# Performance work log

Hardware: AMD Instinct MI355X
Metric: run time of the kernel (lower is better)

## Reference

```python
import jax, jax.numpy as jnp
import numpy as np

NUM_HEADS = 16
EMBED_DIM = 1024
HEAD_SIZE = EMBED_DIM // NUM_HEADS


def setup_inputs() -> dict:
    key = jax.random.key(0)
    ks = jax.random.split(key, 9)
    B, S, D = 4, 2048, EMBED_DIM
    scale = 1.0 / np.sqrt(D)
    x = jax.random.normal(ks[0], (B, S, D), dtype=jnp.float32)
    Wq = jax.random.normal(ks[1], (D, D), dtype=jnp.float32) * scale
    bq = jnp.zeros((D,), dtype=jnp.float32)
    Wk = jax.random.normal(ks[2], (D, D), dtype=jnp.float32) * scale
    bk = jnp.zeros((D,), dtype=jnp.float32)
    Wv = jax.random.normal(ks[3], (D, D), dtype=jnp.float32) * scale
    bv = jnp.zeros((D,), dtype=jnp.float32)
    Wo = jax.random.normal(ks[4], (D, D), dtype=jnp.float32) * scale
    bo = jnp.zeros((D,), dtype=jnp.float32)
    return {"x": x, "Wq": Wq, "bq": bq, "Wk": Wk, "bk": bk,
            "Wv": Wv, "bv": bv, "Wo": Wo, "bo": bo}


def reference(x, Wq, bq, Wk, bk, Wv, bv, Wo, bo):
    B, S, D = x.shape
    H, Hd = NUM_HEADS, HEAD_SIZE

    def split_heads(t):  # [B,S,D] -> [B,H,S,Hd]
        return t.reshape(B, S, H, Hd).transpose(0, 2, 1, 3)

    q = split_heads(x @ Wq + bq)
    k = split_heads(x @ Wk + bk)
    v = split_heads(x @ Wv + bv)

    scores = jnp.einsum("bhqd,bhkd->bhqk", q, k) / np.sqrt(Hd)
    probs = jax.nn.softmax(scores, axis=-1)  # dropout rate=0 -> identity
    ctx = jnp.einsum("bhqk,bhkd->bhqd", probs, v)
    ctx = ctx.transpose(0, 2, 1, 3).reshape(B, S, D)
    return ctx @ Wo + bo
```

## Files before the change

kernel.cpp:

```cpp
#include <hip/hip_runtime.h>
#include <cstdint>


typedef unsigned short ushort_t;
typedef __attribute__((ext_vector_type(8))) short short8;
typedef __attribute__((ext_vector_type(4))) float f32x4;

constexpr int Bn = 4, Sn = 2048, Dn = 1024, Hn = 16;
constexpr int Mn = Bn * Sn;
constexpr float QSCALE = 0.125f * 1.44269504088896340736f;

__device__ __forceinline__ ushort_t f2b(float f) {
    union { float f; unsigned u; } v; v.f = f;
    unsigned u = v.u;
    return (ushort_t)((u + 0x7fffu + ((u >> 16) & 1u)) >> 16);
}

__device__ __forceinline__ unsigned cvt_pk_bf16(float lo, float hi) {
    unsigned r;
    asm("v_cvt_pk_bf16_f32 %0, %1, %2" : "=v"(r) : "v"(lo), "v"(hi));
    return r;
}

__device__ __forceinline__ float exp2_hw(float x) {
    float y;
    asm("v_exp_f32 %0, %1" : "=v"(y) : "v"(x));
    return y;
}

__device__ __forceinline__ void gl_lds16(const void* g, void* l) {
    __builtin_amdgcn_global_load_lds(
        (const __attribute__((address_space(1))) unsigned int*)g,
        (__attribute__((address_space(3))) unsigned int*)l, 16, 0, 0);
}

__global__ void cast_f32_bf16(const float* __restrict__ in, ushort_t* __restrict__ out, int n4) {
    int i = blockIdx.x * blockDim.x + threadIdx.x;
    if (i < n4) {
        float4 f = ((const float4*)in)[i];
        ushort4 o;
        o.x = f2b(f.x); o.y = f2b(f.y); o.z = f2b(f.z); o.w = f2b(f.w);
        ((ushort4*)out)[i] = o;
    }
}

__global__ void transpose_cast_w4(
    const float* __restrict__ W0, const float* __restrict__ W1,
    const float* __restrict__ W2, const float* __restrict__ W3,
    ushort_t* __restrict__ T0, ushort_t* __restrict__ T1,
    ushort_t* __restrict__ T2, ushort_t* __restrict__ T3, int dim) {
    __shared__ float tile[32][33];
    int z = blockIdx.z;
    const float* W = z == 0 ? W0 : (z == 1 ? W1 : (z == 2 ? W2 : W3));
    ushort_t* Wt = z == 0 ? T0 : (z == 1 ? T1 : (z == 2 ? T2 : T3));
    int bx = blockIdx.x * 32;
    int by = blockIdx.y * 32;
    int tx = threadIdx.x, ty = threadIdx.y;
    for (int i = 0; i < 32; i += 8)
        tile[ty + i][tx] = W[(size_t)(by + ty + i) * dim + bx + tx];
    __syncthreads();
    for (int i = 0; i < 32; i += 8)
        Wt[(size_t)(bx + ty + i) * dim + by + tx] = f2b(tile[tx][ty + i]);
}

template <int OUTF32, int QKVSEL>
__global__ __launch_bounds__(256) void gemm_bt(
    const ushort_t* __restrict__ A, const ushort_t* __restrict__ Bt,
    const float* __restrict__ b0, const float* __restrict__ b1, const float* __restrict__ b2,
    void* __restrict__ Cv, ushort_t* __restrict__ Vt,
    int Mq, int Nq, int Kq, float osc0, int nbx) {
    alignas(16) __shared__ ushort_t Al[128 * 64];
    alignas(16) __shared__ ushort_t Bl[128 * 64];
    const int tid = threadIdx.x;
    const int l = tid & 63, wid = tid >> 6;
    const int lo = l & 15, g = l >> 4;
    const int wm = wid >> 1, wn = wid & 1;
    const int per_xcd = (int)gridDim.x >> 3;
    const int virt = ((int)blockIdx.x & 7) * per_xcd + ((int)blockIdx.x >> 3);
    const int m0 = (virt / nbx) * 128, n0g = (virt % nbx) * 128;
    int sel = QKVSEL ? (n0g >> 10) : 0;
    const float* bias = QKVSEL ? (sel == 0 ? b0 : (sel == 1 ? b1 : b2)) : b0;
    float oscale = (QKVSEL && sel != 0) ? 1.0f : osc0;
    const int n0 = QKVSEL ? (n0g & 1023) : n0g;

    const int rr = l >> 3, cc = l & 7;

    f32x4 acc[4][4];
    for (int a = 0; a < 4; ++a)
        for (int b = 0; b < 4; ++b) acc[a][b] = f32x4{0.f, 0.f, 0.f, 0.f};

    for (int kt = 0; kt < Kq; kt += 64) {
        __syncthreads();
#pragma unroll
        for (int i = 0; i < 4; ++i) {
            int row = wid * 32 + i * 8 + rr;
            gl_lds16(&A[(size_t)(m0 + row) * Kq + kt + cc * 8], &Al[(wid * 32 + i * 8) * 64]);
            gl_lds16(&Bt[(size_t)(n0g + row) * Kq + kt + cc * 8], &Bl[(wid * 32 + i * 8) * 64]);
        }
        __syncthreads();
#pragma unroll
        for (int ks = 0; ks < 2; ++ks) {
            short8 af[4], bf[4];
#pragma unroll
            for (int mi = 0; mi < 4; ++mi)
                af[mi] = *(const short8*)&Al[(wm * 64 + mi * 16 + lo) * 64 + ks * 32 + g * 8];
#pragma unroll
            for (int ni = 0; ni < 4; ++ni)
                bf[ni] = *(const short8*)&Bl[(wn * 64 + ni * 16 + lo) * 64 + ks * 32 + g * 8];
            __builtin_amdgcn_s_setprio(1);
#pragma unroll
            for (int mi = 0; mi < 4; ++mi)
#pragma unroll
                for (int ni = 0; ni < 4; ++ni)
                    acc[mi][ni] = __builtin_amdgcn_mfma_f32_16x16x32_bf16(af[mi], bf[ni], acc[mi][ni], 0, 0, 0);
            __builtin_amdgcn_s_setprio(0);
        }
    }
    for (int mi = 0; mi < 4; ++mi) {
        int row = m0 + wm * 64 + mi * 16 + g * 4;
        for (int ni = 0; ni < 4; ++ni) {
            int col = n0 + wn * 64 + ni * 16 + lo;
            float bcol = bias ? bias[col] : 0.f;
            float v0 = (acc[mi][ni][0] + bcol) * oscale;
            float v1 = (acc[mi][ni][1] + bcol) * oscale;
            float v2 = (acc[mi][ni][2] + bcol) * oscale;
            float v3 = (acc[mi][ni][3] + bcol) * oscale;
            if (OUTF32) {
                ((float*)Cv)[(size_t)(row + 0) * Nq + col] = v0;
                ((float*)Cv)[(size_t)(row + 1) * Nq + col] = v1;
                ((float*)Cv)[(size_t)(row + 2) * Nq + col] = v2;
                ((float*)Cv)[(size_t)(row + 3) * Nq + col] = v3;
            } else if (QKVSEL && sel == 2) {
                size_t drow = (size_t)((((unsigned)row >> 11) << 4) + ((unsigned)col >> 6)) * 64 + (col & 63);
                uint2 w;
                w.x = cvt_pk_bf16(v0, v1);
                w.y = cvt_pk_bf16(v2, v3);
                *(uint2*)&Vt[drow * Sn + (row & 2047)] = w;
            } else {
                ushort_t* out = (ushort_t*)Cv + (size_t)sel * Mn * Dn;
                out[(size_t)(row + 0) * Nq + col] = f2b(v0);
                out[(size_t)(row + 1) * Nq + col] = f2b(v1);
                out[(size_t)(row + 2) * Nq + col] = f2b(v2);
                out[(size_t)(row + 3) * Nq + col] = f2b(v3);
            }
        }
    }
}

__global__ __launch_bounds__(256, 2) void attn_kernel(
    const ushort_t* __restrict__ Qg, const ushort_t* __restrict__ Kg,
    const ushort_t* __restrict__ Vtg, ushort_t* __restrict__ Ctx) {
    alignas(16) __shared__ ushort_t Kl[2][64 * 64];
    alignas(16) __shared__ ushort_t Vl[2][64 * 64];
    alignas(16) __shared__ ushort_t Pl[4][64 * 64];
    const int tid = threadIdx.x;
    const int l = tid & 63, wid = tid >> 6;
    const int lo = l & 15, g = l >> 4;
    const int virt = (blockIdx.x & 7) * 64 + (blockIdx.x >> 3);
    const int bh = virt >> 3, qc = virt & 7;
    const int b = bh >> 4, h = bh & 15;
    const int q0 = qc * 256 + wid * 64;
    constexpr int NT = Sn / 64;

    short8 qf[4][2];
#pragma unroll
    for (int qi = 0; qi < 4; ++qi) {
        size_t qrow = (size_t)(b * Sn + q0 + qi * 16 + lo);
#pragma unroll
        for (int ks = 0; ks < 2; ++ks)
            qf[qi][ks] = *(const short8*)&Qg[qrow * Dn + h * 64 + ks * 32 + g * 8];
    }

    const int rr = l >> 3, cc = l & 7;
    const int swc = ((cc ^ rr) << 4);
    const char* gK = (const char*)(Kg + (size_t)(b * Sn) * Dn + h * 64);
    const char* gV = (const char*)(Vtg + (size_t)(bh * 64) * Sn);

    float ls[4] = {0.f, 0.f, 0.f, 0.f};
    f32x4 ctx[4][4];
#pragma unroll
    for (int qi = 0; qi < 4; ++qi)
#pragma unroll
        for (int ni = 0; ni < 4; ++ni) ctx[qi][ni] = f32x4{0.f, 0.f, 0.f, 0.f};

    char* Pw = (char*)Pl[wid];

#define STAGE_KV(T, BUF)                                                                 \
    {                                                                                    \
        int row = wid * 8 + rr;                                                          \
        gl_lds16(gK + ((size_t)((T)*64 + row) * Dn) * 2 + swc,                           \
                 &Kl[BUF][(wid * 8) * 64]);                                              \
        gl_lds16(gK + ((size_t)((T)*64 + row + 32) * Dn) * 2 + swc,                      \
                 &Kl[BUF][(wid * 8 + 32) * 64]);                                         \
        gl_lds16(gV + ((size_t)row * Sn + (size_t)(T)*64) * 2 + swc,                     \
                 &Vl[BUF][(wid * 8) * 64]);                                              \
        gl_lds16(gV + ((size_t)(row + 32) * Sn + (size_t)(T)*64) * 2 + swc,              \
                 &Vl[BUF][(wid * 8 + 32) * 64]);                                         \
    }

    STAGE_KV(0, 0);

    for (int t = 0; t < NT; ++t) {
        const char* Kb = (const char*)Kl[t & 1];
        const char* Vb = (const char*)Vl[t & 1];
        asm volatile("s_waitcnt vmcnt(0)" ::: "memory");
        __builtin_amdgcn_s_barrier();
        __builtin_amdgcn_sched_barrier(0);
        if (t + 1 < NT) STAGE_KV(t + 1, (t + 1) & 1);

        f32x4 sa[4][4];
#pragma unroll
        for (int qi = 0; qi < 4; ++qi)
#pragma unroll
            for (int ni = 0; ni < 4; ++ni) sa[qi][ni] = f32x4{0.f, 0.f, 0.f, 0.f};
#pragma unroll
        for (int ks = 0; ks < 2; ++ks) {
            short8 kf[4];
#pragma unroll
            for (int ni = 0; ni < 4; ++ni) {
                int row = ni * 16 + lo;
                kf[ni] = *(const short8*)(Kb + ((row * 128 + ks * 64 + g * 16) ^ ((lo & 7) << 4)));
            }
            __builtin_amdgcn_s_setprio(1);
#pragma unroll
            for (int qi = 0; qi < 4; ++qi)
#pragma unroll
                for (int ni = 0; ni < 4; ++ni)
                    sa[qi][ni] = __builtin_amdgcn_mfma_f32_16x16x32_bf16(kf[ni], qf[qi][ks], sa[qi][ni], 0, 0, 0);
            __builtin_amdgcn_s_setprio(0);
        }

        short8 vf[2][4];
#pragma unroll
        for (int ks = 0; ks < 2; ++ks)
#pragma unroll
            for (int ni = 0; ni < 4; ++ni) {
                int row = ni * 16 + lo;
                vf[ks][ni] = *(const short8*)(Vb + ((row * 128 + ks * 64 + g * 16) ^ ((lo & 7) << 4)));
            }

#pragma unroll
        for (int qi = 0; qi < 4; ++qi) {
            float r0 = 0.f, r1 = 0.f, r2 = 0.f, r3 = 0.f;
#pragma unroll
            for (int i = 0; i < 4; ++i) {
                sa[qi][0][i] = exp2_hw(sa[qi][0][i]); r0 += sa[qi][0][i];
                sa[qi][1][i] = exp2_hw(sa[qi][1][i]); r1 += sa[qi][1][i];
                sa[qi][2][i] = exp2_hw(sa[qi][2][i]); r2 += sa[qi][2][i];
                sa[qi][3][i] = exp2_hw(sa[qi][3][i]); r3 += sa[qi][3][i];
            }
            ls[qi] += (r0 + r1) + (r2 + r3);
#pragma unroll
            for (int ni = 0; ni < 4; ++ni) {
                uint2 w;
                w.x = cvt_pk_bf16(sa[qi][ni][0], sa[qi][ni][1]);
                w.y = cvt_pk_bf16(sa[qi][ni][2], sa[qi][ni][3]);
                unsigned byte = (unsigned)(((qi * 16 + lo) * 128 + (ni * 16 + g * 4) * 2) ^ ((lo & 7) << 4));
                *(uint2*)(Pw + byte) = w;
            }
        }
        asm volatile("s_waitcnt lgkmcnt(0)" ::: "memory");
        __builtin_amdgcn_sched_barrier(0);

        short8 pa[4][2];
#pragma unroll
        for (int qi = 0; qi < 4; ++qi)
#pragma unroll
            for (int ks = 0; ks < 2; ++ks)
                pa[qi][ks] = *(const short8*)(Pw + (((qi * 16 + lo) * 128 + ks * 64 + g * 16) ^ ((lo & 7) << 4)));
        __builtin_amdgcn_s_setprio(1);
#pragma unroll
        for (int ks = 0; ks < 2; ++ks)
#pragma unroll
            for (int qi = 0; qi < 4; ++qi)
#pragma unroll
                for (int ni = 0; ni < 4; ++ni)
                    ctx[qi][ni] = __builtin_amdgcn_mfma_f32_16x16x32_bf16(pa[qi][ks], vf[ks][ni], ctx[qi][ni], 0, 0, 0);
        __builtin_amdgcn_s_setprio(0);
    }
#undef STAGE_KV

#pragma unroll
    for (int qi = 0; qi < 4; ++qi) {
        float lsum = ls[qi];
        lsum += __shfl_xor(lsum, 16);
        lsum += __shfl_xor(lsum, 32);
        float linv = 1.0f / lsum;
#pragma unroll
        for (int i = 0; i < 4; ++i) {
            float lrow = __shfl(linv, g * 4 + i);
            int prow = qi * 16 + g * 4 + i;
#pragma unroll
            for (int ni = 0; ni < 4; ++ni) {
                unsigned byte = (unsigned)((prow * 128 + (ni * 16 + lo) * 2) ^ ((prow & 7) << 4));
                *(ushort_t*)(Pw + byte) = f2b(ctx[qi][ni][i] * lrow);
            }
        }
    }
    asm volatile("s_waitcnt lgkmcnt(0)" ::: "memory");
    __builtin_amdgcn_sched_barrier(0);
#pragma unroll
    for (int j = 0; j < 8; ++j) {
        int row = j * 8 + rr;
        uint4 w = *(const uint4*)(Pw + ((row * 128 + cc * 16) ^ ((row & 7) << 4)));
        *(uint4*)&Ctx[(size_t)(b * Sn + q0 + row) * Dn + h * 64 + cc * 8] = w;
    }
}

extern "C" void kernel_launch(void* const* d_in, const int* in_sizes, int n_in,
                              void* d_out, int out_size, void* d_ws, size_t ws_size,
                              hipStream_t stream) {
    const float* x  = (const float*)d_in[0];
    const float* Wq = (const float*)d_in[1];
    const float* bq = (const float*)d_in[2];
    const float* Wk = (const float*)d_in[3];
    const float* bk = (const float*)d_in[4];
    const float* Wv = (const float*)d_in[5];
    const float* bv = (const float*)d_in[6];
    const float* Wo = (const float*)d_in[7];
    const float* bo = (const float*)d_in[8];

    ushort_t* ws = (ushort_t*)d_ws;
    const size_t MD = (size_t)Mn * Dn;
    const size_t DD = (size_t)Dn * Dn;
    ushort_t* xb  = ws;
    ushort_t* wqt = xb + MD;
    ushort_t* wkt = wqt + DD;
    ushort_t* wvt = wkt + DD;
    ushort_t* wot = wvt + DD;
    ushort_t* qb  = wot + DD;
    ushort_t* kb  = qb + MD;
    ushort_t* vb  = kb + MD;
    ushort_t* vt  = vb + MD;
    ushort_t* cx  = vt + MD;

    int n4 = (int)(MD / 4);
    cast_f32_bf16<<<(n4 + 255) / 256, 256, 0, stream>>>(x, xb, n4);
    transpose_cast_w4<<<dim3(Dn / 32, Dn / 32, 4), dim3(32, 8), 0, stream>>>(
        Wq, Wk, Wv, Wo, wqt, wkt, wvt, wot, Dn);
    gemm_bt<0, 1><<<dim3(1536), 256, 0, stream>>>(
        xb, wqt, bq, bk, bv, qb, vt, Mn, Dn, Dn, QSCALE, 24);
    attn_kernel<<<dim3(512), 256, 0, stream>>>(qb, kb, vt, cx);
    gemm_bt<1, 0><<<dim3(512), 256, 0, stream>>>(
        cx, wot, bo, nullptr, nullptr, (float*)d_out, nullptr, Mn, Dn, Dn, 1.0f, 8);
}
```

Measured before the change: 197.7 us.

## Software-pipeline QK^T of next KV tile with softmax and PV of current tile

Restructures the attention inner loop so that the QK^T MFMAs and V-fragment loads for tile t+1 are issued between the exp/bf16-pack of tile t and its PV MFMAs. The loop is manually unrolled by two with ping-pong score and V-fragment register sets, and KV prefetch is moved two tiles ahead. The aim is to overlap transcendental/VALU softmax work with matrix-core work and hide the LDS latency that the old serial per-tile schedule exposed. In exchange it doubles the live score accumulators and V fragments, which raises VGPR pressure and may reduce occupancy or cause spills. It also assumes NT is even.

Measured after the change: 638.4 us. 223% more time.

```diff
diff --git a/kernel.cpp b/kernel.cpp
--- a/kernel.cpp
+++ b/kernel.cpp
@@ -185,6 +185,9 @@
 
     char* Pw = (char*)Pl[wid];
 
+    f32x4 sa0[4][4], sa1[4][4];
+    short8 vf0[2][4], vf1[2][4];
+
 #define STAGE_KV(T, BUF)                                                                 \
     {                                                                                    \
         int row = wid * 8 + rr;                                                          \
@@ -198,86 +201,103 @@
                  &Vl[BUF][(wid * 8 + 32) * 64]);                                         \
     }
 
+#define QK_VF(BUF, SAN, VFN)                                                             \
+    {                                                                                    \
+        const char* Kb_ = (const char*)Kl[BUF];                                          \
+        const char* Vb_ = (const char*)Vl[BUF];                                          \
+        _Pragma("unroll")                                                                \
+        for (int qi = 0; qi < 4; ++qi)                                                   \
+            _Pragma("unroll")                                                            \
+            for (int ni = 0; ni < 4; ++ni) SAN[qi][ni] = f32x4{0.f, 0.f, 0.f, 0.f};      \
+        _Pragma("unroll")                                                                \
+        for (int ks = 0; ks < 2; ++ks) {                                                 \
+            short8 kf[4];                                                                \
+            _Pragma("unroll")                                                            \
+            for (int ni = 0; ni < 4; ++ni) {                                             \
+                int row = ni * 16 + lo;                                                  \
+                kf[ni] = *(const short8*)(Kb_ + ((row * 128 + ks * 64 + g * 16) ^ ((lo & 7) << 4))); \
+            }                                                                            \
+            __builtin_amdgcn_s_setprio(1);                                               \
+            _Pragma("unroll")                                                            \
+            for (int qi = 0; qi < 4; ++qi)                                               \
+                _Pragma("unroll")                                                        \
+                for (int ni = 0; ni < 4; ++ni)                                           \
+                    SAN[qi][ni] = __builtin_amdgcn_mfma_f32_16x16x32_bf16(kf[ni], qf[qi][ks], SAN[qi][ni], 0, 0, 0); \
+            __builtin_amdgcn_s_setprio(0);                                               \
+        }                                                                                \
+        _Pragma("unroll")                                                                \
+        for (int ks = 0; ks < 2; ++ks)                                                   \
+            _Pragma("unroll")                                                            \
+            for (int ni = 0; ni < 4; ++ni) {                                             \
+                int row = ni * 16 + lo;                                                  \
+                VFN[ks][ni] = *(const short8*)(Vb_ + ((row * 128 + ks * 64 + g * 16) ^ ((lo & 7) << 4))); \
+            }                                                                            \
+    }
+
+#define BODY(T, SAC, VFC, SAN, VFN, CB, NB)                                              \
+    {                                                                                    \
+                          \
+        _Pragma("unroll")                                                                \
+        for (int qi = 0; qi < 4; ++qi) {                                                 \
+            float r0 = 0.f, r1 = 0.f, r2 = 0.f, r3 = 0.f;                                \
+            _Pragma("unroll")                                                            \
+            for (int i = 0; i < 4; ++i) {                                                \
+                SAC[qi][0][i] = exp2_hw(SAC[qi][0][i]); r0 += SAC[qi][0][i];             \
+                SAC[qi][1][i] = exp2_hw(SAC[qi][1][i]); r1 += SAC[qi][1][i];             \
+                SAC[qi][2][i] = exp2_hw(SAC[qi][2][i]); r2 += SAC[qi][2][i];             \
+                SAC[qi][3][i] = exp2_hw(SAC[qi][3][i]); r3 += SAC[qi][3][i];             \
+            }                                                                            \
+            ls[qi] += (r0 + r1) + (r2 + r3);                                             \
+            _Pragma("unroll")                                                            \
+            for (int ni = 0; ni < 4; ++ni) {                                             \
+                uint2 w;                                                                 \
+                w.x = cvt_pk_bf16(SAC[qi][ni][0], SAC[qi][ni][1]);                       \
+                w.y = cvt_pk_bf16(SAC[qi][ni][2], SAC[qi][ni][3]);                       \
+                unsigned byte = (unsigned)(((qi * 16 + lo) * 128 + (ni * 16 + g * 4) * 2) ^ ((lo & 7) << 4)); \
+                *(uint2*)(Pw + byte) = w;                                                \
+            }                                                                            \
+        }                                                                                \
+        if ((T) + 1 < NT) {                                                              \
+            asm volatile("s_waitcnt vmcnt(0)" ::: "memory");      \
+            __builtin_amdgcn_s_barrier();     \
+            __builtin_amdgcn_sched_barrier(0);                                           \
+            if ((T) + 2 < NT) STAGE_KV((T) + 2, CB);                                     \
+            QK_VF(NB, SAN, VFN);                                  \
+        }                                                                                \
+                  \
+        asm volatile("s_waitcnt lgkmcnt(0)" ::: "memory");                               \
+        __builtin_amdgcn_sched_barrier(0);                                               \
+        short8 pa[4][2];                                                                 \
+        _Pragma("unroll")                                                                \
+        for (int qi = 0; qi < 4; ++qi)                                                   \
+            _Pragma("unroll")                                                            \
+            for (int ks = 0; ks < 2; ++ks)                                               \
+                pa[qi][ks] = *(const short8*)(Pw + (((qi * 16 + lo) * 128 + ks * 64 + g * 16) ^ ((lo & 7) << 4))); \
+        __builtin_amdgcn_s_setprio(1);                                                   \
+        _Pragma("unroll")                                                                \
+        for (int ks = 0; ks < 2; ++ks)                                                   \
+            _Pragma("unroll")                                                            \
+            for (int qi = 0; qi < 4; ++qi)                                               \
+                _Pragma("unroll")                                                        \
+                for (int ni = 0; ni < 4; ++ni)                                           \
+                    ctx[qi][ni] = __builtin_amdgcn_mfma_f32_16x16x32_bf16(pa[qi][ks], VFC[ks][ni], ctx[qi][ni], 0, 0, 0); \
+        __builtin_amdgcn_s_setprio(0);                                                   \
+    }
+
     STAGE_KV(0, 0);
-
-    for (int t = 0; t < NT; ++t) {
-        const char* Kb = (const char*)Kl[t & 1];
-        const char* Vb = (const char*)Vl[t & 1];
-        asm volatile("s_waitcnt vmcnt(0)" ::: "memory");
-        __builtin_amdgcn_s_barrier();
-        __builtin_amdgcn_sched_barrier(0);
-        if (t + 1 < NT) STAGE_KV(t + 1, (t + 1) & 1);
-
-        f32x4 sa[4][4];
-#pragma unroll
-        for (int qi = 0; qi < 4; ++qi)
-#pragma unroll
-            for (int ni = 0; ni < 4; ++ni) sa[qi][ni] = f32x4{0.f, 0.f, 0.f, 0.f};
-#pragma unroll
-        for (int ks = 0; ks < 2; ++ks) {
-            short8 kf[4];
-#pragma unroll
-            for (int ni = 0; ni < 4; ++ni) {
-                int row = ni * 16 + lo;
-                kf[ni] = *(const short8*)(Kb + ((row * 128 + ks * 64 + g * 16) ^ ((lo & 7) << 4)));
-            }
-            __builtin_amdgcn_s_setprio(1);
-#pragma unroll
-            for (int qi = 0; qi < 4; ++qi)
-#pragma unroll
-                for (int ni = 0; ni < 4; ++ni)
-                    sa[qi][ni] = __builtin_amdgcn_mfma_f32_16x16x32_bf16(kf[ni], qf[qi][ks], sa[qi][ni], 0, 0, 0);
-            __builtin_amdgcn_s_setprio(0);
-        }
-
-        short8 vf[2][4];
-#pragma unroll
-        for (int ks = 0; ks < 2; ++ks)
-#pragma unroll
-            for (int ni = 0; ni < 4; ++ni) {
-                int row = ni * 16 + lo;
-                vf[ks][ni] = *(const short8*)(Vb + ((row * 128 + ks * 64 + g * 16) ^ ((lo & 7) << 4)));
-            }
-
-#pragma unroll
-        for (int qi = 0; qi < 4; ++qi) {
-            float r0 = 0.f, r1 = 0.f, r2 = 0.f, r3 = 0.f;
-#pragma unroll
-            for (int i = 0; i < 4; ++i) {
-                sa[qi][0][i] = exp2_hw(sa[qi][0][i]); r0 += sa[qi][0][i];
-                sa[qi][1][i] = exp2_hw(sa[qi][1][i]); r1 += sa[qi][1][i];
-                sa[qi][2][i] = exp2_hw(sa[qi][2][i]); r2 += sa[qi][2][i];
-                sa[qi][3][i] = exp2_hw(sa[qi][3][i]); r3 += sa[qi][3][i];
-            }
-            ls[qi] += (r0 + r1) + (r2 + r3);
-#pragma unroll
-            for (int ni = 0; ni < 4; ++ni) {
-                uint2 w;
-                w.x = cvt_pk_bf16(sa[qi][ni][0], sa[qi][ni][1]);
-                w.y = cvt_pk_bf16(sa[qi][ni][2], sa[qi][ni][3]);
-                unsigned byte = (unsigned)(((qi * 16 + lo) * 128 + (ni * 16 + g * 4) * 2) ^ ((lo & 7) << 4));
-                *(uint2*)(Pw + byte) = w;
-            }
-        }
-        asm volatile("s_waitcnt lgkmcnt(0)" ::: "memory");
-        __builtin_amdgcn_sched_barrier(0);
-
-        short8 pa[4][2];
-#pragma unroll
-        for (int qi = 0; qi < 4; ++qi)
-#pragma unroll
-            for (int ks = 0; ks < 2; ++ks)
-                pa[qi][ks] = *(const short8*)(Pw + (((qi * 16 + lo) * 128 + ks * 64 + g * 16) ^ ((lo & 7) << 4)));
-        __builtin_amdgcn_s_setprio(1);
-#pragma unroll
-        for (int ks = 0; ks < 2; ++ks)
-#pragma unroll
-            for (int qi = 0; qi < 4; ++qi)
-#pragma unroll
-                for (int ni = 0; ni < 4; ++ni)
-                    ctx[qi][ni] = __builtin_amdgcn_mfma_f32_16x16x32_bf16(pa[qi][ks], vf[ks][ni], ctx[qi][ni], 0, 0, 0);
-        __builtin_amdgcn_s_setprio(0);
-    }
+    asm volatile("s_waitcnt vmcnt(0)" ::: "memory");
+    __builtin_amdgcn_s_barrier();
+    STAGE_KV(1, 1);
+    QK_VF(0, sa0, vf0);
+    asm volatile("s_waitcnt lgkmcnt(0)" ::: "memory");
+    __builtin_amdgcn_sched_barrier(0);
+
+    for (int tt = 0; tt < NT; tt += 2) {
+        BODY(tt,     sa0, vf0, sa1, vf1, 0, 1);
+        BODY(tt + 1, sa1, vf1, sa0, vf0, 1, 0);
+    }
+#undef BODY
+#undef QK_VF
 #undef STAGE_KV
 
 #pragma unroll
```
